# Kernel tuning notes

Hardware: AMD Instinct MI355X
Metric: run time of the kernel (lower is better)

The kernel has to match this reference:

```python
import jax, jax.numpy as jnp
import numpy as np

M = 50000
N = 50000
H = 32
C = 128
K = 15          # sum(shell_sizes) = 1 + 14
GROUPS = 8
CPG = C // GROUPS  # 16
RADIUS = 1.2
SIGMA = 0.9
INF = 1.0e6


def _make_kernel_points():
    # fixed='center': first point at origin, rest uniformly in the ball of radius RADIUS
    rng = np.random.RandomState(42)
    pts = rng.randn(K, 3).astype(np.float32)
    pts /= np.linalg.norm(pts, axis=1, keepdims=True) + 1e-9
    r = rng.rand(K, 1).astype(np.float32) ** (1.0 / 3.0)
    pts = pts * r * RADIUS
    pts[0] = 0.0
    return jnp.asarray(pts)


def setup_inputs() -> dict:
    key = jax.random.key(0)
    ks = jax.random.split(key, 8)
    q_pts = jax.random.normal(ks[0], (M, 3), jnp.float32) * 5.0
    s_pts = q_pts + 0.0  # M == N case (same point set)
    s_feats = jax.random.normal(ks[1], (N, C), jnp.float32)
    neighb_inds = jax.random.randint(ks[2], (M, H), 0, N)
    da_scale = jax.random.uniform(ks[3], (M,), jnp.float32, 0.5, 1.5)
    # learned params
    weights = jax.random.normal(ks[4], (K, C), jnp.float32) * (1.0 / np.sqrt(C))
    w1 = jax.random.normal(ks[5], (C, C), jnp.float32) * (1.0 / np.sqrt(C))
    b1 = jnp.zeros((C,), jnp.float32)
    w2 = jax.random.normal(ks[6], (C, K * CPG), jnp.float32) * (1.0 / np.sqrt(C))
    kernel_points = _make_kernel_points()
    return {
        "q_pts": q_pts, "s_pts": s_pts, "s_feats": s_feats,
        "neighb_inds": neighb_inds, "da_scale": da_scale,
        "weights": weights, "w1": w1, "b1": b1, "w2": w2,
        "kernel_points": kernel_points,
    }


def reference(q_pts, s_pts, s_feats, neighb_inds, da_scale,
              weights, w1, b1, w2, kernel_points):
    # --- neighbor feature gather (padded shadow row of zeros) ---
    padded = jnp.concatenate([s_feats, jnp.zeros((1, C), s_feats.dtype)], axis=0)
    neighbor_feats = padded[neighb_inds]               # [M, H, C]

    # --- modulations from pooled feats (M == N -> pooled = s_feats) ---
    pooled = s_feats
    h = jax.nn.leaky_relu(pooled @ w1 + b1, 0.1)
    modulations = jax.nn.sigmoid(h @ w2)               # [M, K*CPG]
    modulations = modulations.reshape(-1, K, CPG, 1)
    conv_w = weights.reshape(1, K, CPG, GROUPS) * modulations
    conv_w = conv_w.reshape(-1, K, C)                  # [M, K, C]

    # --- density-adaptive kernel-point influences (no-grad in original) ---
    s_pad = jnp.concatenate([s_pts, jnp.full((1, 3), INF, s_pts.dtype)], axis=0)
    neighbors = s_pad[neighb_inds] - q_pts[:, None, :]            # [M, H, 3]
    scaled_kp = kernel_points[None] * da_scale[:, None, None]     # [M, K, 3]
    diff = neighbors[:, :, None, :] - scaled_kp[:, None, :, :]    # [M, H, K, 3]
    sq_d = jnp.sum(diff * diff, axis=-1)                          # [M, H, K]
    nn_sq = jnp.min(sq_d, axis=2)                                 # [M, H]
    nn_idx = jnp.argmin(sq_d, axis=2)                             # [M, H]
    infl = jnp.clip(1.0 - jnp.sqrt(nn_sq) / SIGMA, 0.0)           # linear mode
    infl = jax.lax.stop_gradient(infl)

    # --- gather per-neighbor kernel weights, modulate, aggregate ---
    nw = jnp.take_along_axis(conv_w, nn_idx[:, :, None], axis=1)  # [M, H, C]
    nw = nw * infl[:, :, None]
    return jnp.sum(neighbor_feats * nw, axis=1)                   # [M, C]
```

## Files before the change

### kernel.cpp

```cpp
#include <hip/hip_runtime.h>
#include <cstddef>
#include <cstdint>

namespace {
constexpr int H_N    = 32;
constexpr int C_F    = 128;
constexpr int K_P    = 15;
constexpr int MODC   = 240;
constexpr int ROWS_B = 64;
constexpr int LDS_SZ = ROWS_B * MODC * 2;
constexpr int QB     = 96;
}

typedef __attribute__((ext_vector_type(8))) short short8v;
typedef __attribute__((ext_vector_type(4))) float f32x4;

__device__ __forceinline__ unsigned short bf16_hi(float f) {
    unsigned u = __builtin_bit_cast(unsigned, f);
    unsigned r = (u + 0x7FFFu + ((u >> 16) & 1u)) >> 16;
    return (unsigned short)r;
}
__device__ __forceinline__ float bf16_f(unsigned short h) {
    unsigned u = ((unsigned)h) << 16;
    return __builtin_bit_cast(float, u);
}

__global__ __launch_bounds__(256)
void split_w_kernel(const float* __restrict__ w1, const float* __restrict__ w2,
                    unsigned short* __restrict__ w1t, unsigned short* __restrict__ w2t,
                    int* __restrict__ counter)
{
    const int i = blockIdx.x * 256 + threadIdx.x;
    if (i == 0) *counter = 0;
    if (i < C_F * C_F) {
        const int c = i >> 7, j = i & 127;
        w1t[j * C_F + c] = bf16_hi(w1[i]);
    }
    const int i2 = i - C_F * C_F;
    if (i2 >= 0 && i2 < C_F * MODC) {
        const int c = i2 / MODC, j = i2 - c * MODC;
        w2t[j * C_F + c] = bf16_hi(w2[i2]);
    }
}

__global__ __launch_bounds__(512, 2)
void geom_kernel(const float* __restrict__ q_pts,
                 const float* __restrict__ s_pts,
                 const int* __restrict__ nbi,
                 const float* __restrict__ da_scale,
                 const float* __restrict__ kp,
                 int* __restrict__ counter,
                 int* __restrict__ qidx,
                 unsigned* __restrict__ pk,
                 float* __restrict__ gfl,
                 float* __restrict__ out,
                 int M)
{
    __shared__ int      qidx_l[QB];
    __shared__ unsigned pk_l [QB * H_N];
    __shared__ float    gfl_l[QB * H_N];
    __shared__ int cnt_l, base_l;

    const int t    = threadIdx.x;
    const int wave = t >> 6, lane = t & 63;
    const int hl   = lane & 31;
    const int half = lane >> 5;
    const int q0   = blockIdx.x * QB;

    if (t == 0) cnt_l = 0;
    __syncthreads();

    for (int pass = 0; pass < 6; ++pass) {
        const int ql = q0 + pass * 16 + wave * 2 + half;
        const bool valid = ql < M;

        int   idx = 0, nn = 0;
        float fl  = 0.f;
        if (valid) {
            const float qx = q_pts[ql * 3 + 0];
            const float qy = q_pts[ql * 3 + 1];
            const float qz = q_pts[ql * 3 + 2];
            const float das = da_scale[ql];
            idx = nbi[(size_t)ql * H_N + hl];
            const float sx = s_pts[idx * 3 + 0];
            const float sy = s_pts[idx * 3 + 1];
            const float sz = s_pts[idx * 3 + 2];
            const float dx = __fsub_rn(sx, qx);
            const float dy = __fsub_rn(sy, qy);
            const float dz = __fsub_rn(sz, qz);
            const float dd = __fadd_rn(__fadd_rn(__fmul_rn(dx, dx), __fmul_rn(dy, dy)),
                                       __fmul_rn(dz, dz));
            const float reach = 0.9f + 1.2f * das;
            if (dd < reach * reach) {
                float best = 3.4e38f; int bi = 0;
                #pragma unroll
                for (int k = 0; k < K_P; ++k) {
                    const float ex = __fsub_rn(dx, __fmul_rn(kp[k * 3 + 0], das));
                    const float ey = __fsub_rn(dy, __fmul_rn(kp[k * 3 + 1], das));
                    const float ez = __fsub_rn(dz, __fmul_rn(kp[k * 3 + 2], das));
                    const float d2 = __fadd_rn(__fadd_rn(__fmul_rn(ex, ex), __fmul_rn(ey, ey)),
                                               __fmul_rn(ez, ez));
                    if (d2 < best) { best = d2; bi = k; }
                }
                const float f = 1.f - sqrtf(best) / 0.9f;
                fl = fmaxf(f, 0.f);
                nn = bi;
            }
        }

        const unsigned long long mask = __ballot(fl > 0.f);
        const unsigned long long mymask = half ? (mask & 0xFFFFFFFF00000000ull)
                                               : (mask & 0x00000000FFFFFFFFull);
        if (valid && mymask == 0ull) {
            *reinterpret_cast<float4*>(out + (size_t)ql * C_F + hl * 4) =
                make_float4(0.f, 0.f, 0.f, 0.f);
        } else if (valid) {
            int slot = 0;
            if (hl == 0) slot = atomicAdd(&cnt_l, 1);
            slot = __shfl(slot, half * 32);
            if (hl == 0) qidx_l[slot] = ql;
            pk_l [slot * H_N + hl] = (unsigned)idx | ((unsigned)nn << 20);
            gfl_l[slot * H_N + hl] = fl;
        }
    }
    __syncthreads();

    if (t == 0) base_l = atomicAdd(counter, cnt_l);
    __syncthreads();
    const int base = base_l, cnt = cnt_l;

    for (int i = t; i < cnt; i += 512) qidx[base + i] = qidx_l[i];
    for (int i = t; i < cnt * H_N; i += 512) {
        pk [(size_t)base * H_N + i] = pk_l[i];
        gfl[(size_t)base * H_N + i] = gfl_l[i];
    }
}

__global__ __launch_bounds__(512, 4)
void mlp_active_kernel(const float* __restrict__ s_feats,
                       const unsigned short* __restrict__ w1t,
                       const unsigned short* __restrict__ w2t,
                       const float* __restrict__ b1,
                       const int* __restrict__ counter,
                       const int* __restrict__ qidx,
                       unsigned short* __restrict__ modc)
{
    __shared__ __align__(16) unsigned char lds[LDS_SZ];

    const int count = *counter;
    const int r0 = blockIdx.x * ROWS_B;
    const int rows = min(count - r0, ROWS_B);
    if (rows <= 0) return;

    const int t = threadIdx.x;

    {
        const int row = t >> 3;
        const int k0  = (t & 7) << 4;
        const int src_m = (row < rows) ? qidx[r0 + row] : 0;
        const float4* src = reinterpret_cast<const float4*>(
            s_feats + (size_t)src_m * C_F + k0);
        #pragma unroll
        for (int s = 0; s < 2; ++s) {
            float v[8];
            if (row < rows) {
                const float4 a = src[s * 2 + 0];
                const float4 b = src[s * 2 + 1];
                v[0] = a.x; v[1] = a.y; v[2] = a.z; v[3] = a.w;
                v[4] = b.x; v[5] = b.y; v[6] = b.z; v[7] = b.w;
            } else {
                #pragma unroll
                for (int e = 0; e < 8; ++e) v[e] = 0.f;
            }
            short8v hv;
            #pragma unroll
            for (int e = 0; e < 8; ++e) hv[e] = (short)bf16_hi(v[e]);
            const unsigned addr = (unsigned)((row * 256 + (k0 + s * 8) * 2) ^ ((row & 7) << 4));
            *reinterpret_cast<short8v*>(lds + addr) = hv;
        }
    }
    __syncthreads();

    const int wave = t >> 6, lane = t & 63;
    const int wc = wave;
    const int g  = lane >> 4;
    const int ln = lane & 15;

    {
        const int col = wc * 16 + ln;
        f32x4 acc[4];
        {
            const float b = b1[col];
            #pragma unroll
            for (int rt = 0; rt < 4; ++rt) acc[rt] = f32x4{b, b, b, b};
        }
        #pragma unroll
        for (int ks = 0; ks < 4; ++ks) {
            short8v a[4];
            #pragma unroll
            for (int rt = 0; rt < 4; ++rt) {
                const int row = rt * 16 + ln;
                const unsigned addr = (unsigned)((row * 256 + (ks * 32 + g * 8) * 2) ^ ((row & 7) << 4));
                a[rt] = *reinterpret_cast<const short8v*>(lds + addr);
            }
            const short8v b = *reinterpret_cast<const short8v*>(
                w1t + (size_t)col * C_F + ks * 32 + g * 8);
            #pragma unroll
            for (int rt = 0; rt < 4; ++rt)
                acc[rt] = __builtin_amdgcn_mfma_f32_16x16x32_bf16(a[rt], b, acc[rt], 0, 0, 0);
        }
        __syncthreads();

        #pragma unroll
        for (int rt = 0; rt < 4; ++rt) {
            #pragma unroll
            for (int r = 0; r < 4; ++r) {
                float v = acc[rt][r];
                v = v > 0.f ? v : 0.1f * v;
                const int row = rt * 16 + g * 4 + r;
                const unsigned addr = (unsigned)((row * 256 + col * 2) ^ ((row & 7) << 4));
                *reinterpret_cast<unsigned short*>(lds + addr) = bf16_hi(v);
            }
        }
    }
    __syncthreads();

    f32x4 acc2[4][2];
    #pragma unroll
    for (int rt = 0; rt < 4; ++rt)
        #pragma unroll
        for (int cs = 0; cs < 2; ++cs) acc2[rt][cs] = f32x4{0.f, 0.f, 0.f, 0.f};

    #pragma unroll
    for (int ks = 0; ks < 4; ++ks) {
        short8v a[4];
        #pragma unroll
        for (int rt = 0; rt < 4; ++rt) {
            const int row = rt * 16 + ln;
            const unsigned addr = (unsigned)((row * 256 + (ks * 32 + g * 8) * 2) ^ ((row & 7) << 4));
            a[rt] = *reinterpret_cast<const short8v*>(lds + addr);
        }
        #pragma unroll
        for (int cs = 0; cs < 2; ++cs) {
            const int ctile = wc + 8 * cs;
            if (ctile < K_P) {
                const int col = ctile * 16 + ln;
                const short8v b = *reinterpret_cast<const short8v*>(
                    w2t + (size_t)col * C_F + ks * 32 + g * 8);
                #pragma unroll
                for (int rt = 0; rt < 4; ++rt)
                    acc2[rt][cs] = __builtin_amdgcn_mfma_f32_16x16x32_bf16(a[rt], b, acc2[rt][cs], 0, 0, 0);
            }
        }
    }
    #pragma unroll
    for (int rt = 0; rt < 4; ++rt)
        #pragma unroll
        for (int cs = 0; cs < 2; ++cs)
            #pragma unroll
            for (int r = 0; r < 4; ++r)
                acc2[rt][cs][r] = 1.f / (1.f + __expf(-acc2[rt][cs][r]));

    __syncthreads();

    #pragma unroll
    for (int rt = 0; rt < 4; ++rt) {
        #pragma unroll
        for (int cs = 0; cs < 2; ++cs) {
            const int ctile = wc + 8 * cs;
            if (ctile < K_P) {
                const int col = ctile * 16 + ln;
                #pragma unroll
                for (int r = 0; r < 4; ++r) {
                    const int row = rt * 16 + g * 4 + r;
                    *reinterpret_cast<unsigned short*>(
                        lds + row * (MODC * 2) + col * 2) = bf16_hi(acc2[rt][cs][r]);
                }
            }
        }
    }
    __syncthreads();

    for (int gi = t; gi < rows * 30; gi += 512) {
        const int row = gi / 30, u = gi - row * 30;
        const short8v v = *reinterpret_cast<const short8v*>(lds + row * (MODC * 2) + u * 16);
        *reinterpret_cast<short8v*>(modc + (size_t)(r0 + row) * MODC + u * 8) = v;
    }
}

__global__ __launch_bounds__(256)
void gather_kernel(const float* __restrict__ s_feats,
                   const float* __restrict__ weights,
                   const int* __restrict__ counter,
                   const int* __restrict__ qidx,
                   const unsigned* __restrict__ pk,
                   const float* __restrict__ gfl,
                   const unsigned short* __restrict__ modc,
                   float* __restrict__ out)
{
    const int count = *counter;
    if (blockIdx.x * 8 >= count) return;

    const int t    = threadIdx.x;
    const int lane = t & 63;
    const int hl   = lane & 31;
    const int half = lane >> 5;
    const int p    = blockIdx.x * 8 + (t >> 5);
    const bool valid = p < count;

    int   idx = 0, nn = 0;
    float fl  = 0.f;
    if (valid) {
        const unsigned r = pk[(size_t)p * H_N + hl];
        idx = (int)(r & 0xFFFFFu);
        nn  = (int)(r >> 20);
        fl  = gfl[(size_t)p * H_N + hl];
    }

    const unsigned long long mask = __ballot(fl > 0.f);
    unsigned long long mymask = half ? (mask & 0xFFFFFFFF00000000ull)
                                     : (mask & 0x00000000FFFFFFFFull);
    const int c0 = hl << 2;
    float4 acc = {0.f, 0.f, 0.f, 0.f};
    while (mymask) {
        const int hb = __builtin_ctzll(mymask);
        mymask &= mymask - 1;
        const int   ih = __shfl(idx, hb);
        const int   nh = __shfl(nn, hb);
        const float fh = __shfl(fl, hb);
        const float4 fv = *reinterpret_cast<const float4*>(s_feats + (size_t)ih * C_F + c0);
        const float4 wv = *reinterpret_cast<const float4*>(weights + nh * C_F + c0);
        const float  mv = bf16_f(modc[(size_t)p * MODC + nh * 16 + (hl >> 1)]);
        const float  s  = fh * mv;
        acc.x = fmaf(fv.x * wv.x, s, acc.x);
        acc.y = fmaf(fv.y * wv.y, s, acc.y);
        acc.z = fmaf(fv.z * wv.z, s, acc.z);
        acc.w = fmaf(fv.w * wv.w, s, acc.w);
    }
    if (valid) {
        const int mq = qidx[p];
        *reinterpret_cast<float4*>(out + (size_t)mq * C_F + c0) = acc;
    }
}

extern "C" void kernel_launch(void* const* d_in, const int* in_sizes, int n_in,
                              void* d_out, int out_size, void* d_ws, size_t ws_size,
                              hipStream_t stream)
{
    const float* q_pts  = (const float*)d_in[0];
    const float* s_pts  = (const float*)d_in[1];
    const float* s_feat = (const float*)d_in[2];
    const int*   nbi    = (const int*)d_in[3];
    const float* da     = (const float*)d_in[4];
    const float* wts    = (const float*)d_in[5];
    const float* w1     = (const float*)d_in[6];
    const float* b1     = (const float*)d_in[7];
    const float* w2     = (const float*)d_in[8];
    const float* kp     = (const float*)d_in[9];
    float* out = (float*)d_out;

    const int M = in_sizes[4];

    unsigned short* w1t = (unsigned short*)d_ws;
    unsigned short* w2t = w1t + C_F * C_F;
    size_t off = ((size_t)(C_F * C_F + C_F * MODC) * sizeof(unsigned short) + 255) & ~(size_t)255;
    int* counter = (int*)((char*)d_ws + off);           off += 256;
    int* qidx    = (int*)((char*)d_ws + off);           off += (size_t)M * 4;
    off = (off + 255) & ~(size_t)255;
    unsigned* pk = (unsigned*)((char*)d_ws + off);      off += (size_t)M * H_N * 4;
    float* gfl   = (float*)((char*)d_ws + off);         off += (size_t)M * H_N * 4;
    unsigned short* modc = (unsigned short*)((char*)d_ws + off);

    const int nsplit = (C_F * C_F + C_F * MODC + 255) / 256;
    split_w_kernel<<<dim3(nsplit), 256, 0, stream>>>(w1, w2, w1t, w2t, counter);

    geom_kernel<<<dim3((M + QB - 1) / QB), 512, 0, stream>>>(
        q_pts, s_pts, nbi, da, kp, counter, qidx, pk, gfl, out, M);

    mlp_active_kernel<<<dim3((M + ROWS_B - 1) / ROWS_B), 512, 0, stream>>>(
        s_feat, w1t, w2t, b1, counter, qidx, modc);

    gather_kernel<<<dim3((M + 7) / 8), 256, 0, stream>>>(
        s_feat, wts, counter, qidx, pk, gfl, modc, out);
}
```

Measured before the change: 42.63 us.

## Fuse modulation MLP and gather into one kernel, batch geometry loads

Merges the MLP kernel and the gather kernel so the per-query modulations stay in LDS instead of being written to and reread from global memory. This removes one launch and the modc round-trip. The kernel also preloads the W1/W2 MFMA fragments and the pk/gfl/qidx data into registers early, and lowers launch bounds from 4 to 2 blocks per CU to make room for them. Separately, the geometry kernel now issues all six passes' point and neighbor loads up front to raise memory-level parallelism. The cost is higher register pressure and possibly lower occupancy for the gather phase.

```diff
diff --git a/kernel.cpp b/kernel.cpp
--- a/kernel.cpp
+++ b/kernel.cpp
@@ -70,34 +70,47 @@
     if (t == 0) cnt_l = 0;
     __syncthreads();
 
-    for (int pass = 0; pass < 6; ++pass) {
-        const int ql = q0 + pass * 16 + wave * 2 + half;
-        const bool valid = ql < M;
-
-        int   idx = 0, nn = 0;
-        float fl  = 0.f;
-        if (valid) {
-            const float qx = q_pts[ql * 3 + 0];
-            const float qy = q_pts[ql * 3 + 1];
-            const float qz = q_pts[ql * 3 + 2];
-            const float das = da_scale[ql];
-            idx = nbi[(size_t)ql * H_N + hl];
-            const float sx = s_pts[idx * 3 + 0];
-            const float sy = s_pts[idx * 3 + 1];
-            const float sz = s_pts[idx * 3 + 2];
-            const float dx = __fsub_rn(sx, qx);
-            const float dy = __fsub_rn(sy, qy);
-            const float dz = __fsub_rn(sz, qz);
+    float qx[6], qy[6], qz[6], das[6];
+    int   idx[6];
+    bool  valid[6];
+    #pragma unroll
+    for (int p = 0; p < 6; ++p) {
+        const int ql = q0 + p * 16 + wave * 2 + half;
+        valid[p] = ql < M;
+        const int qc = valid[p] ? ql : 0;
+        qx[p]  = q_pts[qc * 3 + 0];
+        qy[p]  = q_pts[qc * 3 + 1];
+        qz[p]  = q_pts[qc * 3 + 2];
+        das[p] = da_scale[qc];
+        idx[p] = nbi[(size_t)qc * H_N + hl];
+    }
+    float sx[6], sy[6], sz[6];
+    #pragma unroll
+    for (int p = 0; p < 6; ++p) {
+        sx[p] = s_pts[idx[p] * 3 + 0];
+        sy[p] = s_pts[idx[p] * 3 + 1];
+        sz[p] = s_pts[idx[p] * 3 + 2];
+    }
+
+    #pragma unroll
+    for (int p = 0; p < 6; ++p) {
+        const int ql = q0 + p * 16 + wave * 2 + half;
+        int   nn = 0;
+        float fl = 0.f;
+        if (valid[p]) {
+            const float dx = __fsub_rn(sx[p], qx[p]);
+            const float dy = __fsub_rn(sy[p], qy[p]);
+            const float dz = __fsub_rn(sz[p], qz[p]);
             const float dd = __fadd_rn(__fadd_rn(__fmul_rn(dx, dx), __fmul_rn(dy, dy)),
                                        __fmul_rn(dz, dz));
-            const float reach = 0.9f + 1.2f * das;
+            const float reach = 0.9f + 1.2f * das[p];
             if (dd < reach * reach) {
                 float best = 3.4e38f; int bi = 0;
                 #pragma unroll
                 for (int k = 0; k < K_P; ++k) {
-                    const float ex = __fsub_rn(dx, __fmul_rn(kp[k * 3 + 0], das));
-                    const float ey = __fsub_rn(dy, __fmul_rn(kp[k * 3 + 1], das));
-                    const float ez = __fsub_rn(dz, __fmul_rn(kp[k * 3 + 2], das));
+                    const float ex = __fsub_rn(dx, __fmul_rn(kp[k * 3 + 0], das[p]));
+                    const float ey = __fsub_rn(dy, __fmul_rn(kp[k * 3 + 1], das[p]));
+                    const float ez = __fsub_rn(dz, __fmul_rn(kp[k * 3 + 2], das[p]));
                     const float d2 = __fadd_rn(__fadd_rn(__fmul_rn(ex, ex), __fmul_rn(ey, ey)),
                                                __fmul_rn(ez, ez));
                     if (d2 < best) { best = d2; bi = k; }
@@ -111,15 +124,15 @@
         const unsigned long long mask = __ballot(fl > 0.f);
         const unsigned long long mymask = half ? (mask & 0xFFFFFFFF00000000ull)
                                                : (mask & 0x00000000FFFFFFFFull);
-        if (valid && mymask == 0ull) {
+        if (valid[p] && mymask == 0ull) {
             *reinterpret_cast<float4*>(out + (size_t)ql * C_F + hl * 4) =
                 make_float4(0.f, 0.f, 0.f, 0.f);
-        } else if (valid) {
+        } else if (valid[p]) {
             int slot = 0;
             if (hl == 0) slot = atomicAdd(&cnt_l, 1);
             slot = __shfl(slot, half * 32);
             if (hl == 0) qidx_l[slot] = ql;
-            pk_l [slot * H_N + hl] = (unsigned)idx | ((unsigned)nn << 20);
+            pk_l [slot * H_N + hl] = (unsigned)idx[p] | ((unsigned)nn << 20);
             gfl_l[slot * H_N + hl] = fl;
         }
     }
@@ -136,14 +149,17 @@
     }
 }
 
-__global__ __launch_bounds__(512, 4)
-void mlp_active_kernel(const float* __restrict__ s_feats,
-                       const unsigned short* __restrict__ w1t,
-                       const unsigned short* __restrict__ w2t,
-                       const float* __restrict__ b1,
-                       const int* __restrict__ counter,
-                       const int* __restrict__ qidx,
-                       unsigned short* __restrict__ modc)
+__global__ __launch_bounds__(512, 2)
+void active_kernel(const float* __restrict__ s_feats,
+                   const float* __restrict__ weights,
+                   const unsigned short* __restrict__ w1t,
+                   const unsigned short* __restrict__ w2t,
+                   const float* __restrict__ b1,
+                   const int* __restrict__ counter,
+                   const int* __restrict__ qidx,
+                   const unsigned* __restrict__ pk,
+                   const float* __restrict__ gfl,
+                   float* __restrict__ out)
 {
     __shared__ __align__(16) unsigned char lds[LDS_SZ];
 
@@ -153,6 +169,42 @@
     if (rows <= 0) return;
 
     const int t = threadIdx.x;
+    const int wave = t >> 6, lane = t & 63;
+    const int wc = wave;
+    const int g  = lane >> 4;
+    const int ln = lane & 15;
+    const int hl   = lane & 31;
+    const int half = lane >> 5;
+
+    short8v w1f[4];
+    #pragma unroll
+    for (int ks = 0; ks < 4; ++ks)
+        w1f[ks] = *reinterpret_cast<const short8v*>(
+            w1t + (size_t)(wc * 16 + ln) * C_F + ks * 32 + g * 8);
+    short8v w2f[4][2];
+    #pragma unroll
+    for (int ks = 0; ks < 4; ++ks) {
+        #pragma unroll
+        for (int cs = 0; cs < 2; ++cs) {
+            const int ctile = wc + 8 * cs;
+            const int colc = (ctile < K_P ? ctile : 0) * 16 + ln;
+            w2f[ks][cs] = *reinterpret_cast<const short8v*>(
+                w2t + (size_t)colc * C_F + ks * 32 + g * 8);
+        }
+    }
+
+    unsigned pkr[4];
+    float    flr[4];
+    int      qir[4];
+    #pragma unroll
+    for (int i = 0; i < 4; ++i) {
+        const int ql = i * 16 + wave * 2 + half;
+        const bool v = ql < rows;
+        const int pos = r0 + (v ? ql : 0);
+        pkr[i] = pk[(size_t)pos * H_N + hl];
+        flr[i] = v ? gfl[(size_t)pos * H_N + hl] : 0.f;
+        qir[i] = qidx[pos];
+    }
 
     {
         const int row = t >> 3;
@@ -181,11 +233,6 @@
     }
     __syncthreads();
 
-    const int wave = t >> 6, lane = t & 63;
-    const int wc = wave;
-    const int g  = lane >> 4;
-    const int ln = lane & 15;
-
     {
         const int col = wc * 16 + ln;
         f32x4 acc[4];
@@ -203,11 +250,9 @@
                 const unsigned addr = (unsigned)((row * 256 + (ks * 32 + g * 8) * 2) ^ ((row & 7) << 4));
                 a[rt] = *reinterpret_cast<const short8v*>(lds + addr);
             }
-            const short8v b = *reinterpret_cast<const short8v*>(
-                w1t + (size_t)col * C_F + ks * 32 + g * 8);
             #pragma unroll
             for (int rt = 0; rt < 4; ++rt)
-                acc[rt] = __builtin_amdgcn_mfma_f32_16x16x32_bf16(a[rt], b, acc[rt], 0, 0, 0);
+                acc[rt] = __builtin_amdgcn_mfma_f32_16x16x32_bf16(a[rt], w1f[ks], acc[rt], 0, 0, 0);
         }
         __syncthreads();
 
@@ -244,12 +289,9 @@
         for (int cs = 0; cs < 2; ++cs) {
             const int ctile = wc + 8 * cs;
             if (ctile < K_P) {
-                const int col = ctile * 16 + ln;
-                const short8v b = *reinterpret_cast<const short8v*>(
-                    w2t + (size_t)col * C_F + ks * 32 + g * 8);
                 #pragma unroll
                 for (int rt = 0; rt < 4; ++rt)
-                    acc2[rt][cs] = __builtin_amdgcn_mfma_f32_16x16x32_bf16(a[rt], b, acc2[rt][cs], 0, 0, 0);
+                    acc2[rt][cs] = __builtin_amdgcn_mfma_f32_16x16x32_bf16(a[rt], w2f[ks][cs], acc2[rt][cs], 0, 0, 0);
             }
         }
     }
@@ -281,65 +323,38 @@
     }
     __syncthreads();
 
-    for (int gi = t; gi < rows * 30; gi += 512) {
-        const int row = gi / 30, u = gi - row * 30;
-        const short8v v = *reinterpret_cast<const short8v*>(lds + row * (MODC * 2) + u * 16);
-        *reinterpret_cast<short8v*>(modc + (size_t)(r0 + row) * MODC + u * 8) = v;
-    }
-}
-
-__global__ __launch_bounds__(256)
-void gather_kernel(const float* __restrict__ s_feats,
-                   const float* __restrict__ weights,
-                   const int* __restrict__ counter,
-                   const int* __restrict__ qidx,
-                   const unsigned* __restrict__ pk,
-                   const float* __restrict__ gfl,
-                   const unsigned short* __restrict__ modc,
-                   float* __restrict__ out)
-{
-    const int count = *counter;
-    if (blockIdx.x * 8 >= count) return;
-
-    const int t    = threadIdx.x;
-    const int lane = t & 63;
-    const int hl   = lane & 31;
-    const int half = lane >> 5;
-    const int p    = blockIdx.x * 8 + (t >> 5);
-    const bool valid = p < count;
-
-    int   idx = 0, nn = 0;
-    float fl  = 0.f;
-    if (valid) {
-        const unsigned r = pk[(size_t)p * H_N + hl];
-        idx = (int)(r & 0xFFFFFu);
-        nn  = (int)(r >> 20);
-        fl  = gfl[(size_t)p * H_N + hl];
-    }
-
-    const unsigned long long mask = __ballot(fl > 0.f);
-    unsigned long long mymask = half ? (mask & 0xFFFFFFFF00000000ull)
-                                     : (mask & 0x00000000FFFFFFFFull);
     const int c0 = hl << 2;
-    float4 acc = {0.f, 0.f, 0.f, 0.f};
-    while (mymask) {
-        const int hb = __builtin_ctzll(mymask);
-        mymask &= mymask - 1;
-        const int   ih = __shfl(idx, hb);
-        const int   nh = __shfl(nn, hb);
-        const float fh = __shfl(fl, hb);
-        const float4 fv = *reinterpret_cast<const float4*>(s_feats + (size_t)ih * C_F + c0);
-        const float4 wv = *reinterpret_cast<const float4*>(weights + nh * C_F + c0);
-        const float  mv = bf16_f(modc[(size_t)p * MODC + nh * 16 + (hl >> 1)]);
-        const float  s  = fh * mv;
-        acc.x = fmaf(fv.x * wv.x, s, acc.x);
-        acc.y = fmaf(fv.y * wv.y, s, acc.y);
-        acc.z = fmaf(fv.z * wv.z, s, acc.z);
-        acc.w = fmaf(fv.w * wv.w, s, acc.w);
-    }
-    if (valid) {
-        const int mq = qidx[p];
-        *reinterpret_cast<float4*>(out + (size_t)mq * C_F + c0) = acc;
+    #pragma unroll
+    for (int i = 0; i < 4; ++i) {
+        const int ql = i * 16 + wave * 2 + half;
+        const bool valid = ql < rows;
+
+        const int   idx = (int)(pkr[i] & 0xFFFFFu);
+        const int   nn  = (int)(pkr[i] >> 20);
+        const float fl  = flr[i];
+
+        const unsigned long long mask = __ballot(fl > 0.f);
+        unsigned long long mymask = half ? (mask & 0xFFFFFFFF00000000ull)
+                                         : (mask & 0x00000000FFFFFFFFull);
+        float4 acc = {0.f, 0.f, 0.f, 0.f};
+        while (mymask) {
+            const int hb = __builtin_ctzll(mymask);
+            mymask &= mymask - 1;
+            const int   ih = __shfl(idx, hb);
+            const int   nh = __shfl(nn, hb);
+            const float fh = __shfl(fl, hb);
+            const float4 fv = *reinterpret_cast<const float4*>(s_feats + (size_t)ih * C_F + c0);
+            const float4 wv = *reinterpret_cast<const float4*>(weights + nh * C_F + c0);
+            const float  mv = bf16_f(*reinterpret_cast<const unsigned short*>(
+                lds + ql * (MODC * 2) + (nh * 16 + (hl >> 1)) * 2));
+            const float  s  = fh * mv;
+            acc.x = fmaf(fv.x * wv.x, s, acc.x);
+            acc.y = fmaf(fv.y * wv.y, s, acc.y);
+            acc.z = fmaf(fv.z * wv.z, s, acc.z);
+            acc.w = fmaf(fv.w * wv.w, s, acc.w);
+        }
+        if (valid)
+            *reinterpret_cast<float4*>(out + (size_t)qir[i] * C_F + c0) = acc;
     }
 }
 
@@ -368,8 +383,7 @@
     int* qidx    = (int*)((char*)d_ws + off);           off += (size_t)M * 4;
     off = (off + 255) & ~(size_t)255;
     unsigned* pk = (unsigned*)((char*)d_ws + off);      off += (size_t)M * H_N * 4;
-    float* gfl   = (float*)((char*)d_ws + off);         off += (size_t)M * H_N * 4;
-    unsigned short* modc = (unsigned short*)((char*)d_ws + off);
+    float* gfl   = (float*)((char*)d_ws + off);
 
     const int nsplit = (C_F * C_F + C_F * MODC + 255) / 256;
     split_w_kernel<<<dim3(nsplit), 256, 0, stream>>>(w1, w2, w1t, w2t, counter);
@@ -377,9 +391,6 @@
     geom_kernel<<<dim3((M + QB - 1) / QB), 512, 0, stream>>>(
         q_pts, s_pts, nbi, da, kp, counter, qidx, pk, gfl, out, M);
 
-    mlp_active_kernel<<<dim3((M + ROWS_B - 1) / ROWS_B), 512, 0, stream>>>(
-        s_feat, w1t, w2t, b1, counter, qidx, modc);
-
-    gather_kernel<<<dim3((M + 7) / 8), 256, 0, stream>>>(
-        s_feat, wts, counter, qidx, pk, gfl, modc, out);
-}
+    active_kernel<<<dim3((M + ROWS_B - 1) / ROWS_B), 512, 0, stream>>>(
+        s_feat, wts, w1t, w2t, b1, counter, qidx, pk, gfl, out);
+}
```

After: 41.76 us. 2.0% less time.
